# Kernel optimization log

Measured on AMD Instinct MI355X. Metric: run time of the kernel, lower is better.

The kernel has to match this reference:

```python
import jax, jax.numpy as jnp
import numpy as np

N_LAYERS = 6
D_T = 6144   # d_transcoder (features per layer)
D_M = 768    # d_model (residual stream)
TOK = 128    # tokens (batch*seq)


def setup_inputs() -> dict:
    key = jax.random.key(0)
    k_x, k_enc, k_dec = jax.random.split(key, 3)
    x = jax.random.normal(k_x, (N_LAYERS, TOK, D_M), jnp.float32)
    W_enc = jax.random.normal(k_enc, (N_LAYERS, D_T, D_M), jnp.float32) * 0.02
    b_enc = jnp.zeros((N_LAYERS, D_T), jnp.float32)
    b_dec = jnp.zeros((N_LAYERS, D_M), jnp.float32)
    # Padded cross-layer decoder: W_dec[i, j] is the decoder from features at
    # layer i writing into layer j's MLP output; only j >= i is valid
    # (original stores a ragged list of [d_transcoder, n_layers - i, d_model]).
    W_dec = jax.random.normal(k_dec, (N_LAYERS, N_LAYERS, D_T, D_M), jnp.float32) * 0.02
    dec_mask = jnp.triu(jnp.ones((N_LAYERS, N_LAYERS), dtype=bool))  # mask[i, j] = (j >= i)
    W_dec = jnp.where(dec_mask[:, :, None, None], W_dec, 0.0)
    return {"x": x, "W_enc": W_enc, "b_enc": b_enc, "b_dec": b_dec,
            "W_dec": W_dec, "dec_mask": dec_mask}


def reference(x, W_enc, b_enc, b_dec, W_dec, dec_mask):
    # Encode: per-layer feature activations [n_layers, tok, d_transcoder]
    acts = jax.nn.relu(jnp.einsum('lnd,lfd->lnf', x, W_enc) + b_enc[:, None, :])
    # Decode: layer-i features write to all layers j >= i (mask enforces triangle)
    Wd = jnp.where(dec_mask[:, :, None, None], W_dec, 0.0)
    recon = jnp.einsum('inf,ijfd->jnd', acts, Wd) + b_dec[:, None, :]
    return recon  # [n_layers, tok, d_model]
```

## Files before the change

### kernel.cpp

```cpp
#include <hip/hip_runtime.h>
#include <hip/hip_bf16.h>

#define NL 6
#define DT 6144
#define DM 768
#define TOK 128

#define EF 32
#define EK 256
#define ENST (DM / EK)

#define TD 256
#define NTD 3

using bf16x8 = __attribute__((ext_vector_type(8))) short;
using f32x4  = __attribute__((ext_vector_type(4))) float;

typedef unsigned int u32;
typedef __attribute__((address_space(1))) const u32 gu32;
typedef __attribute__((address_space(3))) u32 lu32;

__device__ __forceinline__ void stage16(const float* g, float* l) {
  __builtin_amdgcn_global_load_lds((gu32*)g, (lu32*)l, 16, 0, 0);
}

__device__ __forceinline__ short f2bf(float f) {
  union { float f; unsigned u; } c; c.f = f;
  unsigned u = c.u;
  u += 0x7fffu + ((u >> 16) & 1u);
  return (short)(u >> 16);
}

__global__ void initcvt_k(const float* __restrict__ x, ushort* __restrict__ xb) {
  int idx = blockIdx.x * 256 + threadIdx.x;
  if (idx < NL * TOK * DM) xb[idx] = (ushort)f2bf(x[idx]);
}

__global__ __launch_bounds__(256, 2) void encode_k(
    const ushort* __restrict__ xb, const float* __restrict__ W_enc,
    const float* __restrict__ b_enc, ushort* __restrict__ acts)
{
  __shared__ float lw[2][EF][EK];

  const int l  = blockIdx.x / (DT / EF);
  const int f0 = (blockIdx.x % (DT / EF)) * EF;
  const int w    = threadIdx.x >> 6;
  const int lane = threadIdx.x & 63;
  const int lo = lane & 15, hi = lane >> 4;

  const float*  We = W_enc + ((size_t)l * DT + f0) * DM;
  const ushort* Xb = xb + (size_t)l * TOK * DM;

  f32x4 acc[2][2];
  #pragma unroll
  for (int mi = 0; mi < 2; ++mi)
    #pragma unroll
    for (int ni = 0; ni < 2; ++ni)
      acc[mi][ni] = f32x4{0.f, 0.f, 0.f, 0.f};

  #pragma unroll
  for (int q = 0; q < 8; ++q) {
    const int row = w * 8 + q;
    const int g   = lane ^ (row & 7);
    stage16(We + (size_t)row * DM + g * 4, &lw[0][row][0]);
  }
  __syncthreads();

  int cur = 0;
  #pragma unroll 1
  for (int st = 0; st < ENST; ++st) {
    if (st + 1 < ENST) {
      #pragma unroll
      for (int q = 0; q < 8; ++q) {
        const int row = w * 8 + q;
        const int g   = lane ^ (row & 7);
        stage16(We + (size_t)row * DM + (st + 1) * EK + g * 4,
                &lw[cur ^ 1][row][0]);
      }
    }

    const int sw = lo & 7;
    #pragma unroll
    for (int ks = 0; ks < EK / 32; ++ks) {
      bf16x8 a[2], b[2];
      #pragma unroll
      for (int mi = 0; mi < 2; ++mi)
        a[mi] = *(const bf16x8*)(Xb + (size_t)(w * 32 + mi * 16 + lo) * DM
                                 + st * EK + ks * 32 + hi * 8);
      #pragma unroll
      for (int ni = 0; ni < 2; ++ni) {
        const int c0 = (ks * 8 + hi * 2) ^ sw;
        const int c1 = (ks * 8 + hi * 2 + 1) ^ sw;
        const float4 b0 = *(const float4*)&lw[cur][ni * 16 + lo][c0 * 4];
        const float4 b1 = *(const float4*)&lw[cur][ni * 16 + lo][c1 * 4];
        b[ni][0] = f2bf(b0.x); b[ni][1] = f2bf(b0.y);
        b[ni][2] = f2bf(b0.z); b[ni][3] = f2bf(b0.w);
        b[ni][4] = f2bf(b1.x); b[ni][5] = f2bf(b1.y);
        b[ni][6] = f2bf(b1.z); b[ni][7] = f2bf(b1.w);
      }

      #pragma unroll
      for (int mi = 0; mi < 2; ++mi)
        #pragma unroll
        for (int ni = 0; ni < 2; ++ni)
          acc[mi][ni] = __builtin_amdgcn_mfma_f32_16x16x32_bf16(a[mi], b[ni], acc[mi][ni], 0, 0, 0);
    }

    __syncthreads();
    cur ^= 1;
  }

  #pragma unroll
  for (int ni = 0; ni < 2; ++ni) {
    const int f = f0 + ni * 16 + lo;
    const float bias = b_enc[l * DT + f];
    #pragma unroll
    for (int mi = 0; mi < 2; ++mi) {
      #pragma unroll
      for (int rr = 0; rr < 4; ++rr) {
        const int n = w * 32 + mi * 16 + hi * 4 + rr;
        float v = acc[mi][ni][rr] + bias;
        v = v > 0.f ? v : 0.f;
        acts[((size_t)l * TOK + n) * DT + f] = (ushort)f2bf(v);
      }
    }
  }
}

__device__ const int SJ_[6]   = {6, 12, 16, 24, 24, 32};
__device__ const int FJ_[6]   = {1024, 512, 384, 256, 256, 192};
__device__ const int BOFF_[7] = {0, 18, 54, 102, 174, 246, 342};

__global__ __launch_bounds__(256, 2) void decode_k(
    const ushort* __restrict__ acts, const float* __restrict__ W_dec,
    const float* __restrict__ b_dec, float* __restrict__ out)
{
  __shared__ float lw[2][32][TD];

  const int bid = blockIdx.x;
  int j = 0;
  #pragma unroll
  for (int jj = 1; jj < 6; ++jj) if (bid >= BOFF_[jj]) j = jj;
  const int r  = bid - BOFF_[j];
  const int S  = SJ_[j];
  const int F  = FJ_[j];
  const int t  = r / S;
  const int sp = r % S;
  const int fb = sp * F;
  const int ns = F / 32;
  const int nv = (j + 1) * ns;

  const int w = threadIdx.x >> 6;
  const int lane = threadIdx.x & 63;
  const int lo = lane & 15, hi = lane >> 4;

  f32x4 acc[8][4];
  #pragma unroll
  for (int mi = 0; mi < 8; ++mi)
    #pragma unroll
    for (int ni = 0; ni < 4; ++ni)
      acc[mi][ni] = f32x4{0.f, 0.f, 0.f, 0.f};

  {
    const float* W0 = W_dec + ((size_t)(0 * NL + j) * DT + fb) * DM + t * TD;
    #pragma unroll
    for (int q = 0; q < 8; ++q) {
      const int row = w * 8 + q;
      stage16(W0 + (size_t)row * DM + lane * 4, &lw[0][row][0]);
    }
  }
  __syncthreads();

  int cur = 0;
  int i = 0, s = 0;
  #pragma unroll 1
  for (int v = 0; v < nv; ++v) {
    int i2 = i, s2 = s + 1;
    if (s2 == ns) { s2 = 0; ++i2; }

    if (v + 1 < nv) {
      const float* Ws = W_dec + ((size_t)(i2 * NL + j) * DT + fb + s2 * 32) * DM + t * TD;
      #pragma unroll
      for (int q = 0; q < 8; ++q) {
        const int row = w * 8 + q;
        stage16(Ws + (size_t)row * DM + lane * 4, &lw[cur ^ 1][row][0]);
      }
    }

    const ushort* Av = acts + (size_t)i * TOK * DT + fb + s * 32;
    bf16x8 a[8];
    #pragma unroll
    for (int mi = 0; mi < 8; ++mi)
      a[mi] = *(const bf16x8*)(Av + (size_t)(mi * 16 + lo) * DT + hi * 8);

    bf16x8 bb[4];
    #pragma unroll
    for (int ni = 0; ni < 4; ++ni) {
      const int col = w * 64 + ni * 16 + lo;
      #pragma unroll
      for (int e = 0; e < 8; ++e)
        bb[ni][e] = f2bf(lw[cur][hi * 8 + e][col]);
    }

    #pragma unroll
    for (int mi = 0; mi < 8; ++mi)
      #pragma unroll
      for (int ni = 0; ni < 4; ++ni)
        acc[mi][ni] = __builtin_amdgcn_mfma_f32_16x16x32_bf16(a[mi], bb[ni], acc[mi][ni], 0, 0, 0);

    __syncthreads();
    cur ^= 1;
    i = i2; s = s2;
  }

  float* oj = out + (size_t)j * TOK * DM;
  #pragma unroll
  for (int ni = 0; ni < 4; ++ni) {
    const int d = t * TD + w * 64 + ni * 16 + lo;
    const float bias = (sp == 0) ? b_dec[j * DM + d] : 0.f;
    #pragma unroll
    for (int mi = 0; mi < 8; ++mi)
      #pragma unroll
      for (int rr = 0; rr < 4; ++rr)
        atomicAdd(oj + (size_t)(mi * 16 + hi * 4 + rr) * DM + d, acc[mi][ni][rr] + bias);
  }
}

extern "C" void kernel_launch(void* const* d_in, const int* in_sizes, int n_in,
                              void* d_out, int out_size, void* d_ws, size_t ws_size,
                              hipStream_t stream) {
  const float* x     = (const float*)d_in[0];
  const float* W_enc = (const float*)d_in[1];
  const float* b_enc = (const float*)d_in[2];
  const float* b_dec = (const float*)d_in[3];
  const float* W_dec = (const float*)d_in[4];
  float* out = (float*)d_out;
  ushort* acts = (ushort*)d_ws;
  ushort* xb   = acts + (size_t)NL * TOK * DT;

  hipMemsetAsync(out, 0, (size_t)out_size * sizeof(float), stream);
  initcvt_k<<<dim3((NL * TOK * DM + 255) / 256), dim3(256), 0, stream>>>(x, xb);
  encode_k<<<dim3(NL * (DT / EF)), dim3(256), 0, stream>>>(xb, W_enc, b_enc, acts);
  decode_k<<<dim3(342), dim3(256), 0, stream>>>(acts, W_dec, b_dec, out);
}
```

Measured before the change: 201.6 us.

## Split decode per (i,j) layer pair with uniform feature chunks; fold bias init

Decode work is now split into uniform blocks, one per valid (i,j) layer pair, feature chunk of 384 and d-tile, for 1008 blocks. Before, it used 342 blocks with a variable number of steps depending on the target layer. Every block now runs 12 k-steps, which balances load across CUs and improves occupancy. The cost is more blocks doing atomic adds into the output. The output memset is replaced by writing b_dec into the output inside the conversion kernel, which removes a separate memset and the bias logic in decode.

```diff
diff --git a/kernel.cpp b/kernel.cpp
--- a/kernel.cpp
+++ b/kernel.cpp
@@ -12,6 +12,9 @@
 
 #define TD 256
 #define NTD 3
+#define FC 384
+#define NFC 16
+#define NSTEP (FC / 32)
 
 using bf16x8 = __attribute__((ext_vector_type(8))) short;
 using f32x4  = __attribute__((ext_vector_type(4))) float;
@@ -31,9 +34,14 @@
   return (short)(u >> 16);
 }
 
-__global__ void initcvt_k(const float* __restrict__ x, ushort* __restrict__ xb) {
+__global__ void initcvt_k(const float* __restrict__ b_dec,
+                          const float* __restrict__ x,
+                          float* __restrict__ out, ushort* __restrict__ xb) {
   int idx = blockIdx.x * 256 + threadIdx.x;
-  if (idx < NL * TOK * DM) xb[idx] = (ushort)f2bf(x[idx]);
+  if (idx < NL * TOK * DM) {
+    out[idx] = b_dec[(idx / (TOK * DM)) * DM + (idx % DM)];
+    xb[idx] = (ushort)f2bf(x[idx]);
+  }
 }
 
 __global__ __launch_bounds__(256, 2) void encode_k(
@@ -127,32 +135,28 @@
   }
 }
 
-__device__ const int SJ_[6]   = {6, 12, 16, 24, 24, 32};
-__device__ const int FJ_[6]   = {1024, 512, 384, 256, 256, 192};
-__device__ const int BOFF_[7] = {0, 18, 54, 102, 174, 246, 342};
+__device__ const int PI_[21] = {0,0,0,0,0,0, 1,1,1,1,1, 2,2,2,2, 3,3,3, 4,4, 5};
+__device__ const int PJ_[21] = {0,1,2,3,4,5, 1,2,3,4,5, 2,3,4,5, 3,4,5, 4,5, 5};
 
 __global__ __launch_bounds__(256, 2) void decode_k(
     const ushort* __restrict__ acts, const float* __restrict__ W_dec,
-    const float* __restrict__ b_dec, float* __restrict__ out)
+    float* __restrict__ out)
 {
   __shared__ float lw[2][32][TD];
 
   const int bid = blockIdx.x;
-  int j = 0;
-  #pragma unroll
-  for (int jj = 1; jj < 6; ++jj) if (bid >= BOFF_[jj]) j = jj;
-  const int r  = bid - BOFF_[j];
-  const int S  = SJ_[j];
-  const int F  = FJ_[j];
-  const int t  = r / S;
-  const int sp = r % S;
-  const int fb = sp * F;
-  const int ns = F / 32;
-  const int nv = (j + 1) * ns;
-
+  const int p  = bid / (NTD * NFC);
+  const int rm = bid % (NTD * NFC);
+  const int c  = rm / NTD;
+  const int t  = rm % NTD;
+  const int i = PI_[p], j = PJ_[p];
   const int w = threadIdx.x >> 6;
   const int lane = threadIdx.x & 63;
   const int lo = lane & 15, hi = lane >> 4;
+  const int fb = c * FC;
+
+  const float*  Wb = W_dec + ((size_t)(i * NL + j) * DT + fb) * DM + t * TD;
+  const ushort* Ab = acts + (size_t)i * TOK * DT + fb;
 
   f32x4 acc[8][4];
   #pragma unroll
@@ -161,25 +165,18 @@
     for (int ni = 0; ni < 4; ++ni)
       acc[mi][ni] = f32x4{0.f, 0.f, 0.f, 0.f};
 
-  {
-    const float* W0 = W_dec + ((size_t)(0 * NL + j) * DT + fb) * DM + t * TD;
-    #pragma unroll
-    for (int q = 0; q < 8; ++q) {
-      const int row = w * 8 + q;
-      stage16(W0 + (size_t)row * DM + lane * 4, &lw[0][row][0]);
-    }
+  #pragma unroll
+  for (int q = 0; q < 8; ++q) {
+    const int row = w * 8 + q;
+    stage16(Wb + (size_t)row * DM + lane * 4, &lw[0][row][0]);
   }
   __syncthreads();
 
   int cur = 0;
-  int i = 0, s = 0;
   #pragma unroll 1
-  for (int v = 0; v < nv; ++v) {
-    int i2 = i, s2 = s + 1;
-    if (s2 == ns) { s2 = 0; ++i2; }
-
-    if (v + 1 < nv) {
-      const float* Ws = W_dec + ((size_t)(i2 * NL + j) * DT + fb + s2 * 32) * DM + t * TD;
+  for (int s = 0; s < NSTEP; ++s) {
+    if (s + 1 < NSTEP) {
+      const float* Ws = Wb + (size_t)(s + 1) * 32 * DM;
       #pragma unroll
       for (int q = 0; q < 8; ++q) {
         const int row = w * 8 + q;
@@ -187,11 +184,10 @@
       }
     }
 
-    const ushort* Av = acts + (size_t)i * TOK * DT + fb + s * 32;
     bf16x8 a[8];
     #pragma unroll
     for (int mi = 0; mi < 8; ++mi)
-      a[mi] = *(const bf16x8*)(Av + (size_t)(mi * 16 + lo) * DT + hi * 8);
+      a[mi] = *(const bf16x8*)(Ab + (size_t)(mi * 16 + lo) * DT + s * 32 + hi * 8);
 
     bf16x8 bb[4];
     #pragma unroll
@@ -210,19 +206,17 @@
 
     __syncthreads();
     cur ^= 1;
-    i = i2; s = s2;
   }
 
   float* oj = out + (size_t)j * TOK * DM;
   #pragma unroll
   for (int ni = 0; ni < 4; ++ni) {
     const int d = t * TD + w * 64 + ni * 16 + lo;
-    const float bias = (sp == 0) ? b_dec[j * DM + d] : 0.f;
     #pragma unroll
     for (int mi = 0; mi < 8; ++mi)
       #pragma unroll
       for (int rr = 0; rr < 4; ++rr)
-        atomicAdd(oj + (size_t)(mi * 16 + hi * 4 + rr) * DM + d, acc[mi][ni][rr] + bias);
+        atomicAdd(oj + (size_t)(mi * 16 + hi * 4 + rr) * DM + d, acc[mi][ni][rr]);
   }
 }
 
@@ -238,8 +232,7 @@
   ushort* acts = (ushort*)d_ws;
   ushort* xb   = acts + (size_t)NL * TOK * DT;
 
-  hipMemsetAsync(out, 0, (size_t)out_size * sizeof(float), stream);
-  initcvt_k<<<dim3((NL * TOK * DM + 255) / 256), dim3(256), 0, stream>>>(x, xb);
+  initcvt_k<<<dim3((NL * TOK * DM + 255) / 256), dim3(256), 0, stream>>>(b_dec, x, out, xb);
   encode_k<<<dim3(NL * (DT / EF)), dim3(256), 0, stream>>>(xb, W_enc, b_enc, acts);
-  decode_k<<<dim3(342), dim3(256), 0, stream>>>(acts, W_dec, b_dec, out);
-}
+  decode_k<<<dim3(21 * NFC * NTD), dim3(256), 0, stream>>>(acts, W_dec, out);
+}
```

Result: slower. 243.0 us (+20.5%).
